# Kernel tuning notes

Hardware: AMD Instinct MI355X
Metric: run time of the kernel (lower is better)

The kernel has to match this reference:

```python
import jax, jax.numpy as jnp
import numpy as np

E = 40000   # num_entities
R = 474     # num_relations
D = 200     # Config.embedding_dim
L = 100     # n_num_lit
B = 32      # batch

def setup_inputs() -> dict:
    key = jax.random.key(0)
    ks = jax.random.split(key, 11)
    return {
        "e1": jax.random.randint(ks[0], (B, 1), 0, E),
        "rel": jax.random.randint(ks[1], (B, 1), 0, R),
        "emb_e": jax.random.normal(ks[2], (E, D), jnp.float32) * 0.1,           # emb_e.weight
        "emb_rel": jax.random.normal(ks[3], (R, D), jnp.float32) * 0.1,         # emb_rel.weight
        "num_lit": jax.random.normal(ks[4], (E, L), jnp.float32),               # numerical_literals (raw)
        "num_lit_norm": jax.random.uniform(ks[5], (E, L), jnp.float32),         # numerical_literals_normalized
        "W_lit": jax.random.normal(ks[6], (D, D + L), jnp.float32) / np.float32(np.sqrt(D + L)),  # emb_num_lit.weight
        "b_lit": jnp.zeros((D,), jnp.float32),                                  # emb_num_lit.bias
        "c": jax.random.normal(ks[7], (L,), jnp.float32),                       # RBF centers (fixed)
        "var": jax.random.uniform(ks[8], (L,), jnp.float32, minval=0.5, maxval=2.0),  # RBF variances (fixed)
        "nf_w": jax.random.normal(ks[9], (R, L), jnp.float32) * 0.1,            # nf_weights.weight
    }

def reference(e1, rel, emb_e, emb_rel, num_lit, num_lit_norm, W_lit, b_lit, c, var, nf_w):
    e1f = e1.reshape(-1)    # (B,)
    relf = rel.reshape(-1)  # (B,)
    # LiteralE gating via linear layer: emb_num_lit(cat([emb, lit]))
    e1_emb = jnp.concatenate([emb_e[e1f], num_lit_norm[e1f]], axis=1) @ W_lit.T + b_lit  # (B, D)
    e2_multi_emb = jnp.concatenate([emb_e, num_lit_norm], axis=1) @ W_lit.T + b_lit      # (E, D)
    rel_emb = emb_rel[relf]                                                              # (B, D)
    # dropout is identity at inference
    score_l = (e1_emb * rel_emb) @ e2_multi_emb.T  # (B, E)
    # KBLN numerical-literal score: broadcast diff + RBF + weighted reduction over literals
    n = num_lit[e1f][:, None, :] - num_lit[None, :, :]   # (B, E, L) -- large intermediate
    phi = jnp.exp(-jnp.square(n - c) / var)              # RBF, pointwise
    score_n = jnp.einsum('bel,bl->be', phi, nf_w[relf])  # bmm(phi, w_nf^T).squeeze()
    return jax.nn.sigmoid(score_l + score_n)             # (B, E)
```

## Files before the change

kernel.cpp:

```cpp
#include <hip/hip_runtime.h>
#include <math.h>

#define E_N 40000
#define D_N 200
#define L_N 100
#define K_N 300
#define B_N 32

typedef float  f32x4 __attribute__((ext_vector_type(4)));
typedef short  s16x8 __attribute__((ext_vector_type(8)));

#define WS_SH 0
#define WS_W  3200
#define WS_NR 6400
#define WS_S0 6500
#define WS_STAGE 6532
#define WS_PA 6532

__device__ inline float fast_exp2(float x) {
#if __has_builtin(__builtin_amdgcn_exp2f)
    return __builtin_amdgcn_exp2f(x);
#else
    return exp2f(x);
#endif
}
__device__ inline float fast_rcp(float x) {
#if __has_builtin(__builtin_amdgcn_rcpf)
    return __builtin_amdgcn_rcpf(x);
#else
    return 1.0f / x;
#endif
}
__device__ inline ushort f2bf(float f) {
    uint u = __builtin_bit_cast(uint, f);
    u += 0x7fffu + ((u >> 16) & 1u);
    return (ushort)(u >> 16);
}
__device__ inline s16x8 pack_bf8(f32x4 lo, f32x4 hi) {
    s16x8 bb;
    bb[0] = (short)f2bf(lo[0]); bb[1] = (short)f2bf(lo[1]);
    bb[2] = (short)f2bf(lo[2]); bb[3] = (short)f2bf(lo[3]);
    bb[4] = (short)f2bf(hi[0]); bb[5] = (short)f2bf(hi[1]);
    bb[6] = (short)f2bf(hi[2]); bb[7] = (short)f2bf(hi[3]);
    return bb;
}

__global__ __launch_bounds__(320) void prep_kernel(
    const int* __restrict__ e1, const int* __restrict__ rel,
    const float* __restrict__ emb_e, const float* __restrict__ emb_rel,
    const float* __restrict__ num_lit, const float* __restrict__ num_lit_norm,
    const float* __restrict__ W, const float* __restrict__ b_lit,
    const float* __restrict__ c, const float* __restrict__ var,
    const float* __restrict__ nf_w, float* __restrict__ ws)
{
    const int b = blockIdx.x;
    const int t = threadIdx.x;
    __shared__ float q[D_N];
    const int e1b = e1[b];
    const int rb  = rel[b];

    if (t < D_N) {
        const float* wr = W + t * K_N;
        const float* er = emb_e + (long)e1b * D_N;
        const float* nl = num_lit_norm + (long)e1b * L_N;
        float s0_ = b_lit[t], s1_ = 0.f, s2_ = 0.f, s3_ = 0.f;
        for (int k = 0; k < D_N; k += 4) {
            s0_ += er[k+0] * wr[k+0]; s1_ += er[k+1] * wr[k+1];
            s2_ += er[k+2] * wr[k+2]; s3_ += er[k+3] * wr[k+3];
        }
        for (int k = 0; k < L_N; k += 4) {
            s0_ += nl[k+0] * wr[D_N+k+0]; s1_ += nl[k+1] * wr[D_N+k+1];
            s2_ += nl[k+2] * wr[D_N+k+2]; s3_ += nl[k+3] * wr[D_N+k+3];
        }
        q[t] = ((s0_ + s1_) + (s2_ + s3_)) * emb_rel[rb * D_N + t];
    }
    __syncthreads();

    {
        float pk = 0.f;
        if (t < K_N) {
            float a0 = 0.f, a1 = 0.f, a2 = 0.f, a3 = 0.f;
            for (int d = 0; d < D_N; d += 4) {
                a0 += q[d+0] * W[(d+0) * K_N + t];
                a1 += q[d+1] * W[(d+1) * K_N + t];
                a2 += q[d+2] * W[(d+2) * K_N + t];
                a3 += q[d+3] * W[(d+3) * K_N + t];
            }
            pk = (a0 + a1) + (a2 + a3);
        }
        const int s  = t >> 5;
        const int g  = (t >> 3) & 3;
        const int j  = t & 7;
        const int mt = b >> 4;
        const int ln = (g << 4) | (b & 15);
        ushort* pa = (ushort*)(ws + WS_PA);
        pa[((mt * 10 + s) * 64 + ln) * 8 + j] = f2bf(pk);
    }

    if (t < L_N) {
        const float r = sqrtf(1.4426950408889634f / var[t]);
        ws[WS_SH + t * 32 + b] = r * (num_lit[(long)e1b * L_N + t] - c[t]);
        ws[WS_W  + t * 32 + b] = nf_w[rb * L_N + t];
        if (b == 0) ws[WS_NR + t] = -r;
    }
    if (t == 300) {
        float s = 0.f;
        for (int d = 0; d < D_N; ++d) s += q[d] * b_lit[d];
        ws[WS_S0 + b] = s;
    }
}

__global__ __launch_bounds__(256, 4) void score_kernel(
    const float* __restrict__ emb_e, const float* __restrict__ num_lit,
    const float* __restrict__ num_lit_norm, const float* __restrict__ ws,
    float* __restrict__ out)
{
    __shared__ float smem[WS_STAGE];

    const int lane = threadIdx.x & 63;
    const int wv   = threadIdx.x >> 6;
    const int tile = blockIdx.x * 4 + wv;
    const int mt   = tile & 1;
    const int eg   = tile >> 1;
    const int er   = lane & 15;
    const int g    = lane >> 4;
    const int e    = eg * 16 + er;
    const int b0   = mt * 16 + 4 * g;

    {
        const f32x4* s4 = (const f32x4*)ws;
        f32x4* d4 = (f32x4*)smem;
        for (int i = threadIdx.x; i < 1633; i += 256) d4[i] = s4[i];
    }

    f32x4 acc = *(const f32x4*)(ws + WS_S0 + b0);

    s16x8 afr[10];
    {
        const s16x8* pAg = (const s16x8*)(ws + WS_PA);
#pragma unroll
        for (int s = 0; s < 10; ++s) afr[s] = pAg[(mt * 10 + s) * 64 + lane];
    }

    const float* embr = emb_e        + (long)e * D_N;
    const float* litn = num_lit_norm + (long)e * L_N;

#pragma unroll
    for (int s = 0; s < 9; ++s) {
        const int k0 = 32 * s + 8 * g;
        const float* bp = (k0 < 200) ? (embr + k0) : (litn + (k0 - 200));
        f32x4 lo = *(const f32x4*)bp;
        f32x4 hi = *(const f32x4*)(bp + 4);
        acc = __builtin_amdgcn_mfma_f32_16x16x32_bf16(afr[s], pack_bf8(lo, hi), acc, 0, 0, 0);
    }
    {
        f32x4 z = {0.f, 0.f, 0.f, 0.f};
        f32x4 lo = z, hi = z;
        if (g == 0)      { lo = *(const f32x4*)(litn + 88); hi = *(const f32x4*)(litn + 92); }
        else if (g == 1) { lo = *(const f32x4*)(litn + 96); }
        acc = __builtin_amdgcn_mfma_f32_16x16x32_bf16(afr[9], pack_bf8(lo, hi), acc, 0, 0, 0);
    }

    __syncthreads();

    const float* shL = smem + WS_SH;
    const float* wL  = smem + WS_W;
    const float* nrL = smem + WS_NR;

    const f32x4* m4 = (const f32x4*)(num_lit + (long)e * L_N);
    const f32x4* n4 = (const f32x4*)nrL;
    f32x4 mv_a = m4[0];
    f32x4 mv_b = m4[1];
    for (int lc = 0; lc < 25; ++lc) {
        const f32x4 mv = mv_a;
        mv_a = mv_b;
        if (lc + 2 < 25) mv_b = m4[lc + 2];
        f32x4 nv = n4[lc];
#pragma unroll
        for (int ll = 0; ll < 4; ++ll) {
            const int l = lc * 4 + ll;
            const float rm = nv[ll] * mv[ll];
            f32x4 s4 = *(const f32x4*)(shL + l * 32 + b0);
            f32x4 w4 = *(const f32x4*)(wL  + l * 32 + b0);
#pragma unroll
            for (int j = 0; j < 4; ++j) {
                const float u = rm + s4[j];
                acc[j] = fmaf(fast_exp2(-(u * u)), w4[j], acc[j]);
            }
        }
    }

#pragma unroll
    for (int j = 0; j < 4; ++j) {
        const float z = fast_exp2(acc[j] * -1.4426950408889634f);
        out[(long)(b0 + j) * E_N + e] = fast_rcp(1.0f + z);
    }
}

extern "C" void kernel_launch(void* const* d_in, const int* in_sizes, int n_in,
                              void* d_out, int out_size, void* d_ws, size_t ws_size,
                              hipStream_t stream) {
    const int*   e1       = (const int*)d_in[0];
    const int*   rel      = (const int*)d_in[1];
    const float* emb_e    = (const float*)d_in[2];
    const float* emb_rel  = (const float*)d_in[3];
    const float* num_lit  = (const float*)d_in[4];
    const float* num_lit_norm = (const float*)d_in[5];
    const float* W_lit    = (const float*)d_in[6];
    const float* b_lit    = (const float*)d_in[7];
    const float* c        = (const float*)d_in[8];
    const float* var      = (const float*)d_in[9];
    const float* nf_w     = (const float*)d_in[10];
    float* out = (float*)d_out;
    float* ws  = (float*)d_ws;

    hipLaunchKernelGGL(prep_kernel, dim3(B_N), dim3(320), 0, stream,
                       e1, rel, emb_e, emb_rel, num_lit, num_lit_norm,
                       W_lit, b_lit, c, var, nf_w, ws);
    hipLaunchKernelGGL(score_kernel, dim3(1250), dim3(256), 0, stream,
                       emb_e, num_lit, num_lit_norm, ws, out);
}
```

Before: 47.99 us.

## Split K and literal reduction across wave pairs, staging only half the batch

Each block now handles one 16-row batch half, with two waves per entity tile: one takes the first half of the MFMA K-steps and RBF literal chunks, the other takes the rest. Partial accumulators are combined through shared memory before the sigmoid. The grid doubles, and each block stages only its batch half of the shift/weight tables into LDS. This shortens per-wave serial exp work and shrinks the staging copy, at the cost of an extra barrier, an LDS reduction, and reloading A fragments across more blocks.

```diff
diff --git a/kernel.cpp b/kernel.cpp
--- a/kernel.cpp
+++ b/kernel.cpp
@@ -14,8 +14,12 @@
 #define WS_W  3200
 #define WS_NR 6400
 #define WS_S0 6500
-#define WS_STAGE 6532
 #define WS_PA 6532
+
+#define SM_W    1600
+#define SM_NR   3200
+#define SM_CB   3316
+#define SM_TOT  3828
 
 __device__ inline float fast_exp2(float x) {
 #if __has_builtin(__builtin_amdgcn_exp2f)
@@ -115,85 +119,116 @@
     const float* __restrict__ num_lit_norm, const float* __restrict__ ws,
     float* __restrict__ out)
 {
-    __shared__ float smem[WS_STAGE];
+    __shared__ float smem[SM_TOT];
 
     const int lane = threadIdx.x & 63;
     const int wv   = threadIdx.x >> 6;
-    const int tile = blockIdx.x * 4 + wv;
-    const int mt   = tile & 1;
-    const int eg   = tile >> 1;
+    const int wti  = wv & 1;
+    const int h    = wv >> 1;
+    const int mt   = blockIdx.x & 1;
+    const int egp  = blockIdx.x >> 1;
+    const int eg   = egp * 2 + wti;
     const int er   = lane & 15;
     const int g    = lane >> 4;
     const int e    = eg * 16 + er;
-    const int b0   = mt * 16 + 4 * g;
+    const int mt4  = mt * 4;
 
     {
         const f32x4* s4 = (const f32x4*)ws;
         f32x4* d4 = (f32x4*)smem;
-        for (int i = threadIdx.x; i < 1633; i += 256) d4[i] = s4[i];
-    }
-
-    f32x4 acc = *(const f32x4*)(ws + WS_S0 + b0);
-
-    s16x8 afr[10];
+        for (int i = threadIdx.x; i < 829; i += 256) {
+            int src;
+            if (i < 400) {
+                src = (i >> 2) * 8 + mt4 + (i & 3);
+            } else if (i < 800) {
+                const int ii = i - 400;
+                src = 800 + (ii >> 2) * 8 + mt4 + (ii & 3);
+            } else if (i < 825) {
+                src = 1600 + (i - 800);
+            } else {
+                src = 1625 + mt4 + (i - 825);
+            }
+            d4[i] = s4[src];
+        }
+    }
+
+    f32x4 acc = {0.f, 0.f, 0.f, 0.f};
+    if (h == 0) acc = *(const f32x4*)(ws + WS_S0 + mt * 16 + 4 * g);
+
+    s16x8 afr[5];
     {
         const s16x8* pAg = (const s16x8*)(ws + WS_PA);
 #pragma unroll
-        for (int s = 0; s < 10; ++s) afr[s] = pAg[(mt * 10 + s) * 64 + lane];
+        for (int i = 0; i < 5; ++i) afr[i] = pAg[(mt * 10 + h * 5 + i) * 64 + lane];
     }
 
     const float* embr = emb_e        + (long)e * D_N;
     const float* litn = num_lit_norm + (long)e * L_N;
 
 #pragma unroll
-    for (int s = 0; s < 9; ++s) {
-        const int k0 = 32 * s + 8 * g;
+    for (int i = 0; i < 4; ++i) {
+        const int k0 = 32 * (h * 5 + i) + 8 * g;
         const float* bp = (k0 < 200) ? (embr + k0) : (litn + (k0 - 200));
         f32x4 lo = *(const f32x4*)bp;
         f32x4 hi = *(const f32x4*)(bp + 4);
-        acc = __builtin_amdgcn_mfma_f32_16x16x32_bf16(afr[s], pack_bf8(lo, hi), acc, 0, 0, 0);
-    }
-    {
+        acc = __builtin_amdgcn_mfma_f32_16x16x32_bf16(afr[i], pack_bf8(lo, hi), acc, 0, 0, 0);
+    }
+    if (h == 0) {
+        const int k0 = 128 + 8 * g;
+        f32x4 lo = *(const f32x4*)(embr + k0);
+        f32x4 hi = *(const f32x4*)(embr + k0 + 4);
+        acc = __builtin_amdgcn_mfma_f32_16x16x32_bf16(afr[4], pack_bf8(lo, hi), acc, 0, 0, 0);
+    } else {
         f32x4 z = {0.f, 0.f, 0.f, 0.f};
         f32x4 lo = z, hi = z;
         if (g == 0)      { lo = *(const f32x4*)(litn + 88); hi = *(const f32x4*)(litn + 92); }
         else if (g == 1) { lo = *(const f32x4*)(litn + 96); }
-        acc = __builtin_amdgcn_mfma_f32_16x16x32_bf16(afr[9], pack_bf8(lo, hi), acc, 0, 0, 0);
+        acc = __builtin_amdgcn_mfma_f32_16x16x32_bf16(afr[4], pack_bf8(lo, hi), acc, 0, 0, 0);
     }
 
     __syncthreads();
 
-    const float* shL = smem + WS_SH;
-    const float* wL  = smem + WS_W;
-    const float* nrL = smem + WS_NR;
-
+    const float* shT = smem;
+    const float* wT  = smem + SM_W;
+    const f32x4* n4  = (const f32x4*)(smem + SM_NR);
+
+    const int lc0 = h ? 13 : 0;
+    const int lcE = h ? 25 : 13;
     const f32x4* m4 = (const f32x4*)(num_lit + (long)e * L_N);
-    const f32x4* n4 = (const f32x4*)nrL;
-    f32x4 mv_a = m4[0];
-    f32x4 mv_b = m4[1];
-    for (int lc = 0; lc < 25; ++lc) {
+    f32x4 mv_a = m4[lc0];
+    f32x4 mv_b = m4[lc0 + 1];
+    for (int lc = lc0; lc < lcE; ++lc) {
         const f32x4 mv = mv_a;
         mv_a = mv_b;
-        if (lc + 2 < 25) mv_b = m4[lc + 2];
+        if (lc + 2 < lcE) mv_b = m4[lc + 2];
         f32x4 nv = n4[lc];
 #pragma unroll
         for (int ll = 0; ll < 4; ++ll) {
             const int l = lc * 4 + ll;
             const float rm = nv[ll] * mv[ll];
-            f32x4 s4 = *(const f32x4*)(shL + l * 32 + b0);
-            f32x4 w4 = *(const f32x4*)(wL  + l * 32 + b0);
+            f32x4 s4v = *(const f32x4*)(shT + l * 16 + 4 * g);
+            f32x4 w4v = *(const f32x4*)(wT  + l * 16 + 4 * g);
 #pragma unroll
             for (int j = 0; j < 4; ++j) {
-                const float u = rm + s4[j];
-                acc[j] = fmaf(fast_exp2(-(u * u)), w4[j], acc[j]);
+                const float u = rm + s4v[j];
+                acc[j] = fmaf(fast_exp2(-(u * u)), w4v[j], acc[j]);
             }
         }
     }
 
-#pragma unroll
-    for (int j = 0; j < 4; ++j) {
-        const float z = fast_exp2(acc[j] * -1.4426950408889634f);
-        out[(long)(b0 + j) * E_N + e] = fast_rcp(1.0f + z);
+    float* cbuf = smem + SM_CB;
+    if (h) {
+        *(f32x4*)(cbuf + (wti * 64 + lane) * 4) = acc;
+    }
+    __syncthreads();
+    if (!h) {
+        const f32x4 o = *(const f32x4*)(cbuf + (wti * 64 + lane) * 4);
+#pragma unroll
+        for (int j = 0; j < 4; ++j) {
+            const float v = acc[j] + o[j];
+            const float z = fast_exp2(v * -1.4426950408889634f);
+            out[(long)(mt * 16 + 4 * g + j) * E_N + e] = fast_rcp(1.0f + z);
+        }
     }
 }
 
@@ -217,6 +252,6 @@
     hipLaunchKernelGGL(prep_kernel, dim3(B_N), dim3(320), 0, stream,
                        e1, rel, emb_e, emb_rel, num_lit, num_lit_norm,
                        W_lit, b_lit, c, var, nf_w, ws);
-    hipLaunchKernelGGL(score_kernel, dim3(1250), dim3(256), 0, stream,
+    hipLaunchKernelGGL(score_kernel, dim3(2500), dim3(256), 0, stream,
                        emb_e, num_lit, num_lit_norm, ws, out);
 }
```

Measured after the change: 48.82 us. No clear change (+1.7%).
